# Performance work log

Hardware: AMD Instinct MI355X
Metric: run time of the kernel (lower is better)

The kernel has to match this reference:

```python
import jax, jax.numpy as jnp
import numpy as np

MARGIN = 0.3
EPS = 1e-12


def setup_inputs() -> dict:
    key = jax.random.key(0)
    k1, k2 = jax.random.split(key)
    inputs = jax.random.normal(k1, (128, 131072), dtype=jnp.float32)
    targets = jax.random.randint(k2, (128,), 0, 8).astype(jnp.int64)
    return {"inputs": inputs, "targets": targets}


def reference(inputs, targets):
    n = inputs.shape[0]  # 128, hardcoded layout: two modality halves of 64
    # Pairwise Euclidean distance matrix (n, n)
    sq = jnp.sum(inputs * inputs, axis=1, keepdims=True)  # (n, 1)
    dist = sq + sq.T - 2.0 * (inputs @ inputs.T)
    dist = jnp.sqrt(jnp.clip(dist, EPS, None))

    same_label = targets[:, None] == targets[None, :]  # (n, n)
    # modality indicator: first half = modality 0, second half = modality 1
    half = jnp.arange(n) >= (n // 2)
    cross_modality = half[:, None] != half[None, :]  # (n, n)

    # hard positive: same label, opposite modality (mask * mask_modality_final)
    pos_mask = same_label & cross_modality
    # hard negative: where (mask + mask_modality_final_neg) == 0
    # i.e. different label AND opposite modality
    neg_mask = (~same_label) & cross_modality

    neg_inf = jnp.float32(-jnp.inf)
    pos_inf = jnp.float32(jnp.inf)
    dist_ap = jnp.max(jnp.where(pos_mask, dist, neg_inf), axis=1)  # (n,)
    dist_an = jnp.min(jnp.where(neg_mask, dist, pos_inf), axis=1)  # (n,)

    # MarginRankingLoss with y=1: mean(relu(-(dist_an - dist_ap) + margin))
    loss = jnp.mean(jax.nn.relu(dist_ap - dist_an + MARGIN))
    return loss
```

## Files before the change

kernel.cpp:

```cpp
#include <hip/hip_runtime.h>
#include <hip/hip_bf16.h>

typedef __attribute__((ext_vector_type(8))) short bf16x8;
typedef __attribute__((ext_vector_type(4))) float f32x4;

#define N      128
#define KTOT   131072
#define BK     64
#define LDT    (BK + 8)

__device__ __forceinline__ ushort f2bf(float f) {
    union { float f; unsigned u; } v; v.f = f;
    unsigned u = v.u;
    return (ushort)((u + 0x7fffu + ((u >> 16) & 1u)) >> 16);
}

template <bool ATOMIC>
__global__ __launch_bounds__(256) void gram_kernel(const float* __restrict__ X,
                                                   float* __restrict__ out,
                                                   int KC) {
    __shared__ ushort tile[N][LDT];

    const int t    = threadIdx.x;
    const int lane = t & 63;
    const int wv   = t >> 6;
    const int fr   = lane & 15;
    const int fh   = lane >> 4;
    const int c4   = t & 15;
    const int r0   = t >> 4;

    const long kbase = (long)blockIdx.x * (long)KC;

    f32x4 acc[2][8];
#pragma unroll
    for (int i = 0; i < 2; ++i)
#pragma unroll
        for (int j = 0; j < 8; ++j)
            acc[i][j] = (f32x4){0.f, 0.f, 0.f, 0.f};

    const int nstages = KC / BK;
    for (int s = 0; s < nstages; ++s) {
        const long kk = kbase + (long)s * BK;
#pragma unroll
        for (int p = 0; p < 8; ++p) {
            const int row = r0 + p * 16;
            const float4 v = *(const float4*)(X + (long)row * KTOT + kk + c4 * 4);
            ushort4 h;
            h.x = f2bf(v.x); h.y = f2bf(v.y); h.z = f2bf(v.z); h.w = f2bf(v.w);
            *(ushort4*)&tile[row][c4 * 4] = h;
        }
        __syncthreads();

#pragma unroll
        for (int kh = 0; kh < 2; ++kh) {
            bf16x8 bfrag[8];
#pragma unroll
            for (int j = 0; j < 8; ++j)
                bfrag[j] = *(const bf16x8*)&tile[j * 16 + fr][kh * 32 + fh * 8];
#pragma unroll
            for (int i = 0; i < 2; ++i) {
                const bf16x8 afrag = *(const bf16x8*)&tile[(wv * 2 + i) * 16 + fr][kh * 32 + fh * 8];
#pragma unroll
                for (int j = 0; j < 8; ++j)
                    acc[i][j] = __builtin_amdgcn_mfma_f32_16x16x32_bf16(afrag, bfrag[j], acc[i][j], 0, 0, 0);
            }
        }
        __syncthreads();
    }

    if (ATOMIC) {
#pragma unroll
        for (int i = 0; i < 2; ++i)
#pragma unroll
            for (int j = 0; j < 8; ++j)
#pragma unroll
                for (int r = 0; r < 4; ++r) {
                    const int rg = (wv * 2 + i) * 16 + fh * 4 + r;
                    const int cg = j * 16 + fr;
                    atomicAdd(&out[rg * N + cg], acc[i][j][r]);
                }
    } else {
        float* dst = out + (size_t)blockIdx.x * (size_t)(N * N);
#pragma unroll
        for (int i = 0; i < 2; ++i)
#pragma unroll
            for (int j = 0; j < 8; ++j)
#pragma unroll
                for (int r = 0; r < 4; ++r) {
                    const int rg = (wv * 2 + i) * 16 + fh * 4 + r;
                    const int cg = j * 16 + fr;
                    dst[rg * N + cg] = acc[i][j][r];
                }
    }
}

__global__ __launch_bounds__(256) void reduce_kernel(const float* __restrict__ part,
                                                     float* __restrict__ C, int NB) {
    const int j = blockIdx.x * 256 + threadIdx.x;
    float s = 0.f;
#pragma unroll 8
    for (int b = 0; b < NB; ++b)
        s += part[(size_t)b * (size_t)(N * N) + j];
    C[j] = s;
}

__global__ __launch_bounds__(128) void loss_kernel(const float* __restrict__ C,
                                                   const int* __restrict__ tg,
                                                   float* __restrict__ out) {
    __shared__ float Cs[N][N + 4];
    __shared__ float sqs[N];
    __shared__ int   ts[N];
    __shared__ float red[2];

    const int t = threadIdx.x;
#pragma unroll
    for (int it = 0; it < 32; ++it) {
        const int idx = it * 512 + t * 4;
        const float4 v = *(const float4*)(C + idx);
        const int r = idx >> 7;
        const int c = idx & 127;
        Cs[r][c] = v.x; Cs[r][c + 1] = v.y; Cs[r][c + 2] = v.z; Cs[r][c + 3] = v.w;
    }
    ts[t] = tg[t];
    __syncthreads();
    sqs[t] = Cs[t][t];
    __syncthreads();

    const int   ti  = ts[t];
    const int   hi  = t >> 6;
    const float sqi = sqs[t];
    float ap = -INFINITY, an = INFINITY;
#pragma unroll 4
    for (int jj = 0; jj < N; ++jj) {
        const int j = (jj + t) & (N - 1);
        const float d2 = sqi + sqs[j] - 2.0f * Cs[t][j];
        const float d  = sqrtf(fmaxf(d2, 1e-12f));
        const bool cross = ((j >> 6) != hi);
        const bool same  = (ts[j] == ti);
        if (cross && same)  ap = fmaxf(ap, d);
        if (cross && !same) an = fminf(an, d);
    }
    float li = fmaxf(ap - an + 0.3f, 0.0f);

#pragma unroll
    for (int off = 32; off > 0; off >>= 1)
        li += __shfl_down(li, off, 64);
    if ((t & 63) == 0) red[t >> 6] = li;
    __syncthreads();
    if (t == 0) out[0] = (red[0] + red[1]) * (1.0f / (float)N);
}

extern "C" void kernel_launch(void* const* d_in, const int* in_sizes, int n_in,
                              void* d_out, int out_size, void* d_ws, size_t ws_size,
                              hipStream_t stream) {
    const float* X  = (const float*)d_in[0];
    const int*   tg = (const int*)d_in[1];
    float*       out = (float*)d_out;

    const int    NB         = 256;
    const size_t part_elems = (size_t)NB * (size_t)(N * N);
    const size_t need       = (part_elems + (size_t)(N * N)) * sizeof(float);

    if (ws_size >= need) {
        float* part = (float*)d_ws;
        float* C    = part + part_elems;
        gram_kernel<false><<<NB, 256, 0, stream>>>(X, part, KTOT / NB);
        reduce_kernel<<<(N * N) / 256, 256, 0, stream>>>(part, C, NB);
        loss_kernel<<<1, 128, 0, stream>>>(C, tg, out);
    } else {
        float* C = (float*)d_ws;
        hipMemsetAsync(C, 0, (size_t)(N * N) * sizeof(float), stream);
        gram_kernel<true><<<64, 256, 0, stream>>>(X, C, KTOT / 64);
        loss_kernel<<<1, 128, 0, stream>>>(C, tg, out);
    }
}
```

Baseline: 128.0 us.

## Prefetch next K-stage into registers, use 8 waves, and split partial reduction

```diff
diff --git a/kernel.cpp b/kernel.cpp
--- a/kernel.cpp
+++ b/kernel.cpp
@@ -1,24 +1,27 @@
 #include <hip/hip_runtime.h>
 #include <hip/hip_bf16.h>
 
-typedef __attribute__((ext_vector_type(8))) short bf16x8;
-typedef __attribute__((ext_vector_type(4))) float f32x4;
+typedef __attribute__((ext_vector_type(8))) short  bf16x8;
+typedef __attribute__((ext_vector_type(8))) ushort ushortx8;
+typedef __attribute__((ext_vector_type(4))) float  f32x4;
 
-#define N      128
-#define KTOT   131072
-#define BK     64
-#define LDT    (BK + 8)
+#define N     128
+#define KTOT  131072
+#define NB    256
+#define KC    (KTOT / NB)
+#define BK    64
+#define NST   (KC / BK)
+#define LDT   72
 
 __device__ __forceinline__ ushort f2bf(float f) {
     union { float f; unsigned u; } v; v.f = f;
-    unsigned u = v.u;
+    const unsigned u = v.u;
     return (ushort)((u + 0x7fffu + ((u >> 16) & 1u)) >> 16);
 }
 
 template <bool ATOMIC>
-__global__ __launch_bounds__(256) void gram_kernel(const float* __restrict__ X,
-                                                   float* __restrict__ out,
-                                                   int KC) {
+__global__ __launch_bounds__(512) void gram_kernel(const float* __restrict__ X,
+                                                   float* __restrict__ out) {
     __shared__ ushort tile[N][LDT];
 
     const int t    = threadIdx.x;
@@ -26,82 +29,99 @@
     const int wv   = t >> 6;
     const int fr   = lane & 15;
     const int fh   = lane >> 4;
+    const int r0   = t >> 4;
     const int c4   = t & 15;
-    const int r0   = t >> 4;
 
-    const long kbase = (long)blockIdx.x * (long)KC;
+    const long kbase = (long)blockIdx.x * KC;
+    const float* xp = X + kbase + (long)r0 * KTOT + c4 * 4;
 
-    f32x4 acc[2][8];
+    f32x4 acc[8];
 #pragma unroll
-    for (int i = 0; i < 2; ++i)
+    for (int j = 0; j < 8; ++j) acc[j] = (f32x4){0.f, 0.f, 0.f, 0.f};
+
+    float4 rg[4], ng[4];
 #pragma unroll
-        for (int j = 0; j < 8; ++j)
-            acc[i][j] = (f32x4){0.f, 0.f, 0.f, 0.f};
+    for (int p = 0; p < 4; ++p)
+        rg[p] = *(const float4*)(xp + (long)(32 * p) * KTOT);
 
-    const int nstages = KC / BK;
-    for (int s = 0; s < nstages; ++s) {
-        const long kk = kbase + (long)s * BK;
+    auto store_stage = [&]() {
 #pragma unroll
-        for (int p = 0; p < 8; ++p) {
-            const int row = r0 + p * 16;
-            const float4 v = *(const float4*)(X + (long)row * KTOT + kk + c4 * 4);
+        for (int p = 0; p < 4; ++p) {
             ushort4 h;
-            h.x = f2bf(v.x); h.y = f2bf(v.y); h.z = f2bf(v.z); h.w = f2bf(v.w);
-            *(ushort4*)&tile[row][c4 * 4] = h;
+            h.x = f2bf(rg[p].x); h.y = f2bf(rg[p].y);
+            h.z = f2bf(rg[p].z); h.w = f2bf(rg[p].w);
+            *(ushort4*)&tile[r0 + 32 * p][c4 * 4] = h;
         }
-        __syncthreads();
-
+    };
+    auto mfma_stage = [&]() {
 #pragma unroll
         for (int kh = 0; kh < 2; ++kh) {
-            bf16x8 bfrag[8];
+            const bf16x8 af = *(const bf16x8*)&tile[wv * 16 + fr][kh * 32 + fh * 8];
 #pragma unroll
-            for (int j = 0; j < 8; ++j)
-                bfrag[j] = *(const bf16x8*)&tile[j * 16 + fr][kh * 32 + fh * 8];
-#pragma unroll
-            for (int i = 0; i < 2; ++i) {
-                const bf16x8 afrag = *(const bf16x8*)&tile[(wv * 2 + i) * 16 + fr][kh * 32 + fh * 8];
-#pragma unroll
-                for (int j = 0; j < 8; ++j)
-                    acc[i][j] = __builtin_amdgcn_mfma_f32_16x16x32_bf16(afrag, bfrag[j], acc[i][j], 0, 0, 0);
+            for (int j = 0; j < 8; ++j) {
+                const bf16x8 bf = *(const bf16x8*)&tile[j * 16 + fr][kh * 32 + fh * 8];
+                acc[j] = __builtin_amdgcn_mfma_f32_16x16x32_bf16(af, bf, acc[j], 0, 0, 0);
             }
         }
+    };
+
+    for (int s = 0; s < NST - 1; ++s) {
         __syncthreads();
+        store_stage();
+#pragma unroll
+        for (int p = 0; p < 4; ++p)
+            ng[p] = *(const float4*)(xp + (long)(s + 1) * BK + (long)(32 * p) * KTOT);
+        __syncthreads();
+        mfma_stage();
+#pragma unroll
+        for (int p = 0; p < 4; ++p) rg[p] = ng[p];
     }
+    __syncthreads();
+    store_stage();
+    __syncthreads();
+    mfma_stage();
 
     if (ATOMIC) {
 #pragma unroll
-        for (int i = 0; i < 2; ++i)
+        for (int j = 0; j < 8; ++j)
 #pragma unroll
-            for (int j = 0; j < 8; ++j)
-#pragma unroll
-                for (int r = 0; r < 4; ++r) {
-                    const int rg = (wv * 2 + i) * 16 + fh * 4 + r;
-                    const int cg = j * 16 + fr;
-                    atomicAdd(&out[rg * N + cg], acc[i][j][r]);
-                }
+            for (int r = 0; r < 4; ++r)
+                atomicAdd(&out[(wv * 16 + fh * 4 + r) * N + j * 16 + fr], acc[j][r]);
     } else {
         float* dst = out + (size_t)blockIdx.x * (size_t)(N * N);
 #pragma unroll
-        for (int i = 0; i < 2; ++i)
+        for (int j = 0; j < 8; ++j)
 #pragma unroll
-            for (int j = 0; j < 8; ++j)
-#pragma unroll
-                for (int r = 0; r < 4; ++r) {
-                    const int rg = (wv * 2 + i) * 16 + fh * 4 + r;
-                    const int cg = j * 16 + fr;
-                    dst[rg * N + cg] = acc[i][j][r];
-                }
+            for (int r = 0; r < 4; ++r)
+                dst[(wv * 16 + fh * 4 + r) * N + j * 16 + fr] = acc[j][r];
     }
 }
 
 __global__ __launch_bounds__(256) void reduce_kernel(const float* __restrict__ part,
-                                                     float* __restrict__ C, int NB) {
-    const int j = blockIdx.x * 256 + threadIdx.x;
-    float s = 0.f;
+                                                     float* __restrict__ C) {
+    __shared__ float2 red[256];
+    const int t  = threadIdx.x;
+    const int g  = t >> 5;
+    const int jo = t & 31;
+    const size_t jb = (size_t)blockIdx.x * 64;
+
+    float2 s = {0.f, 0.f};
 #pragma unroll 8
-    for (int b = 0; b < NB; ++b)
-        s += part[(size_t)b * (size_t)(N * N) + j];
-    C[j] = s;
+    for (int b = 0; b < 32; ++b) {
+        const float2 v = ((const float2*)(part + (size_t)(g * 32 + b) * (N * N) + jb))[jo];
+        s.x += v.x; s.y += v.y;
+    }
+    red[t] = s;
+    __syncthreads();
+    if (t < 32) {
+        float2 a = red[t];
+#pragma unroll
+        for (int g2 = 1; g2 < 8; ++g2) {
+            const float2 v = red[g2 * 32 + t];
+            a.x += v.x; a.y += v.y;
+        }
+        ((float2*)(C + jb))[t] = a;
+    }
 }
 
 __global__ __launch_bounds__(128) void loss_kernel(const float* __restrict__ C,
@@ -153,24 +173,23 @@
 extern "C" void kernel_launch(void* const* d_in, const int* in_sizes, int n_in,
                               void* d_out, int out_size, void* d_ws, size_t ws_size,
                               hipStream_t stream) {
-    const float* X  = (const float*)d_in[0];
-    const int*   tg = (const int*)d_in[1];
+    const float* X   = (const float*)d_in[0];
+    const int*   tg  = (const int*)d_in[1];
     float*       out = (float*)d_out;
 
-    const int    NB         = 256;
     const size_t part_elems = (size_t)NB * (size_t)(N * N);
     const size_t need       = (part_elems + (size_t)(N * N)) * sizeof(float);
 
     if (ws_size >= need) {
         float* part = (float*)d_ws;
         float* C    = part + part_elems;
-        gram_kernel<false><<<NB, 256, 0, stream>>>(X, part, KTOT / NB);
-        reduce_kernel<<<(N * N) / 256, 256, 0, stream>>>(part, C, NB);
+        gram_kernel<false><<<NB, 512, 0, stream>>>(X, part);
+        reduce_kernel<<<(N * N) / 64, 256, 0, stream>>>(part, C);
         loss_kernel<<<1, 128, 0, stream>>>(C, tg, out);
     } else {
         float* C = (float*)d_ws;
         hipMemsetAsync(C, 0, (size_t)(N * N) * sizeof(float), stream);
-        gram_kernel<true><<<64, 256, 0, stream>>>(X, C, KTOT / 64);
+        gram_kernel<true><<<NB, 512, 0, stream>>>(X, C);
         loss_kernel<<<1, 128, 0, stream>>>(C, tg, out);
     }
 }
```

Measured after the change: 111.1 us. 13.2% less time.
